# Optimization experiments

Hardware: AMD Instinct MI355X
Metric: run time of the kernel (lower is better)

Reference implementation:

```python
import jax, jax.numpy as jnp
import numpy as np

NUM_EMBEDDINGS = 1024
EMBEDDING_DIM = 128
COMMITMENT_COST = 1.0
DECAY = 0.99
EPSILON = 1e-05
N_TOKENS = 65536


def setup_inputs() -> dict:
    key = jax.random.key(0)
    k1, k2, k3 = jax.random.split(key, 3)
    inputs = jax.random.normal(k1, (N_TOKENS, EMBEDDING_DIM), dtype=jnp.float32)
    embedding = jax.random.normal(k2, (NUM_EMBEDDINGS, EMBEDDING_DIM), dtype=jnp.float32) * 0.01
    cluster_size = jnp.ones((NUM_EMBEDDINGS,), dtype=jnp.float32)
    embed_avg = jax.random.normal(k3, (NUM_EMBEDDINGS, EMBEDDING_DIM), dtype=jnp.float32) * 0.01
    return {"inputs": inputs, "embedding": embedding,
            "cluster_size": cluster_size, "embed_avg": embed_avg}


def reference(inputs, embedding, cluster_size, embed_avg):
    # inputs: [N, D], embedding: [K, D]
    flat = inputs.reshape(-1, EMBEDDING_DIM)
    distances = (jnp.sum(flat * flat, axis=1, keepdims=True)
                 + jnp.sum(embedding * embedding, axis=1)
                 - 2.0 * flat @ embedding.T)
    idx = jnp.argmin(distances, axis=1)                       # [N]
    quantized = embedding[idx].reshape(inputs.shape)          # direct gather (same math as one-hot matmul)

    # EMA update (training path); one-hot matmuls replaced by bincount/segment_sum
    dw = jnp.zeros((NUM_EMBEDDINGS,), dtype=flat.dtype).at[idx].add(1.0)   # encodings.sum(0)
    new_cluster_size = cluster_size * DECAY + (1.0 - DECAY) * dw
    dw_embed = jax.ops.segment_sum(flat, idx, num_segments=NUM_EMBEDDINGS)  # encodings.T @ flat
    new_embed_avg = embed_avg * DECAY + (1.0 - DECAY) * dw_embed
    n = jnp.sum(new_cluster_size)
    cs = (new_cluster_size + EPSILON) / (n + NUM_EMBEDDINGS * EPSILON) * n
    new_embedding = new_embed_avg / cs[:, None]

    # losses (quantized/inputs detach semantics are identical values in fwd)
    diff2 = jnp.mean((quantized - inputs) ** 2)
    loss = diff2 + COMMITMENT_COST * diff2

    # straight-through estimator: value equals quantized
    quantized_st = inputs + jax.lax.stop_gradient(quantized - inputs)
    return (quantized_st, loss, idx, new_embedding, new_cluster_size, new_embed_avg)
```

## Files before the change

kernel.cpp:

```cpp
#include <hip/hip_runtime.h>

typedef __attribute__((ext_vector_type(8))) _Float16 half8;
typedef __attribute__((ext_vector_type(4))) float f32x4;

constexpr int NTOK = 65536;
constexpr int DIM  = 128;
constexpr int NK   = 1024;

__global__ void bprep_k(const float* __restrict__ emb, char* __restrict__ bp,
                        float* __restrict__ embT, float* __restrict__ e2s,
                        double* __restrict__ en2d, int* __restrict__ nflag) {
  int i = blockIdx.x * 256 + threadIdx.x;
  if (i == 0) *nflag = 0;
  int c = i >> 4;
  int g = i & 15;
  float4 v0 = *(const float4*)&emb[c * 128 + g * 8];
  float4 v1 = *(const float4*)&emb[c * 128 + g * 8 + 4];
  float vf[8] = {v0.x, v0.y, v0.z, v0.w, v1.x, v1.y, v1.z, v1.w};
  half8 hv;
  double pacc = 0.0;
#pragma unroll
  for (int j = 0; j < 8; j++) {
    hv[j] = (_Float16)vf[j];
    embT[(g * 8 + j) * NK + c] = vf[j];
    pacc = fma((double)vf[j], (double)vf[j], pacc);
  }
  int chunk = c >> 5, n = (c >> 4) & 1, cl = c & 15;
  int kk = g >> 2, lo4 = g & 3;
  *(half8*)(bp + chunk * 8192 + kk * 2048 + n * 1024 + (lo4 * 16 + cl) * 16) = hv;
#pragma unroll
  for (int mask = 1; mask < 16; mask <<= 1) pacc += __shfl_xor(pacc, mask);
  if (g == 0) {
    en2d[c] = pacc;
    e2s[c] = (float)(pacc * 134217728.0 + 1073741824.0);
  }
}

__global__ __launch_bounds__(128, 2)
void argmin_k(const float* __restrict__ x, const char* __restrict__ bp,
              const float* __restrict__ e2s, int* __restrict__ idx_arr,
              float* __restrict__ out_idx, int* __restrict__ nflag,
              int* __restrict__ flags) {
  const int t    = threadIdx.x;
  const int lane = t & 63;
  const int w    = t >> 6;
  const int l15  = lane & 15;
  const int lo4  = lane >> 4;
  const int rbase = blockIdx.x * 64;
  const int lb16 = lane * 16;

  half8 FA[4][2], FB[4][2];

#define LOADG(DST, C, KK)                                                      \
  {                                                                            \
    const char* _b = bp + ((C) * 8192 + (KK) * 2048) + lb16;                   \
    DST[0] = *(const half8*)_b;                                                \
    DST[1] = *(const half8*)(_b + 1024);                                       \
  }

#pragma unroll
  for (int kk = 0; kk < 4; kk++) LOADG(FA[kk], 0, kk)
#pragma unroll
  for (int kk = 0; kk < 4; kk++) LOADG(FB[kk], 1, kk)

  half8 ah[2][4];
#pragma unroll
  for (int m = 0; m < 2; m++)
#pragma unroll
    for (int kk = 0; kk < 4; kk++) {
      const float* xp = &x[(rbase + w * 32 + m * 16 + l15) * 128 + kk * 32 + lo4 * 8];
      float4 v0 = *(const float4*)xp;
      float4 v1 = *(const float4*)(xp + 4);
      float vf[8] = {v0.x, v0.y, v0.z, v0.w, v1.x, v1.y, v1.z, v1.w};
      half8 av;
#pragma unroll
      for (int j = 0; j < 8; j++) av[j] = (_Float16)vf[j];
      ah[m][kk] = av;
    }

  unsigned bv[2][4], b2[2][4];
#pragma unroll
  for (int m = 0; m < 2; m++)
#pragma unroll
    for (int r = 0; r < 4; r++) { bv[m][r] = 0xFFFFFFFFu; b2[m][r] = 0xFFFFFFFFu; }

#define MFMA_PHASE(BANK, KK)                                                   \
  {                                                                            \
    acc[0][0] = __builtin_amdgcn_mfma_f32_16x16x32_f16(ah[0][KK], BANK[KK][0], acc[0][0], 0, 0, 0); \
    acc[1][0] = __builtin_amdgcn_mfma_f32_16x16x32_f16(ah[1][KK], BANK[KK][0], acc[1][0], 0, 0, 0); \
    acc[0][1] = __builtin_amdgcn_mfma_f32_16x16x32_f16(ah[0][KK], BANK[KK][1], acc[0][1], 0, 0, 0); \
    acc[1][1] = __builtin_amdgcn_mfma_f32_16x16x32_f16(ah[1][KK], BANK[KK][1], acc[1][1], 0, 0, 0); \
  }

#define KEY_EPI(C)                                                             \
  {                                                                            \
    _Pragma("unroll")                                                          \
    for (int n = 0; n < 2; n++) {                                              \
      unsigned col = (unsigned)((C) * 32 + n * 16 + l15);                      \
      float e2v = n ? e2b : e2a;                                               \
      _Pragma("unroll")                                                        \
      for (int m = 0; m < 2; m++)                                              \
        _Pragma("unroll")                                                      \
        for (int r = 0; r < 4; r++) {                                          \
          float ks = fmaf(acc[m][n][r], -268435456.0f, e2v);                   \
          unsigned key = ((unsigned)ks & 0xFFFFFC00u) | col;                   \
          unsigned old = bv[m][r];                                             \
          bv[m][r] = min(old, key);                                            \
          b2[m][r] = min(b2[m][r], max(old, key));                             \
        }                                                                      \
    }                                                                          \
  }

  for (int c = 0; c < 32; c += 2) {
    {
      float e2a = e2s[c * 32 + l15];
      float e2b = e2s[c * 32 + 16 + l15];
      f32x4 acc[2][2];
#pragma unroll
      for (int m = 0; m < 2; m++)
#pragma unroll
        for (int n = 0; n < 2; n++) acc[m][n] = (f32x4)(0.0f);
#pragma unroll
      for (int kk = 0; kk < 4; kk++) {
        MFMA_PHASE(FA, kk)
        LOADG(FA[kk], c + 2, kk)
      }
      KEY_EPI(c)
    }
    {
      float e2a = e2s[(c + 1) * 32 + l15];
      float e2b = e2s[(c + 1) * 32 + 16 + l15];
      f32x4 acc[2][2];
#pragma unroll
      for (int m = 0; m < 2; m++)
#pragma unroll
        for (int n = 0; n < 2; n++) acc[m][n] = (f32x4)(0.0f);
#pragma unroll
      for (int kk = 0; kk < 4; kk++) {
        MFMA_PHASE(FB, kk)
        LOADG(FB[kk], c + 3, kk)
      }
      KEY_EPI(c + 1)
    }
  }
#undef LOADG
#undef MFMA_PHASE
#undef KEY_EPI

#pragma unroll
  for (int m = 0; m < 2; m++)
#pragma unroll
    for (int r = 0; r < 4; r++) {
      unsigned v = bv[m][r], v2 = b2[m][r];
      for (int mask = 1; mask < 16; mask <<= 1) {
        unsigned ov = __shfl_xor(v, mask);
        unsigned o2 = __shfl_xor(v2, mask);
        v2 = min(min(v2, o2), max(v, ov));
        v  = min(v, ov);
      }
      if (l15 == 0) {
        int row = rbase + w * 32 + m * 16 + lo4 * 4 + r;
        int ii = (int)(v & 1023u);
        idx_arr[row] = ii;
        out_idx[row] = (float)ii;
        if ((v2 >> 10) - (v >> 10) < 79u) {
          int p = atomicAdd(nflag, 1); flags[p] = row;
        }
      }
    }
}

__global__ __launch_bounds__(256)
void fb_k(const float* __restrict__ x, const float* __restrict__ embT,
          const double* __restrict__ en2d, const int* __restrict__ nflag,
          const int* __restrict__ flags, int* __restrict__ idx_arr,
          float* __restrict__ out_idx) {
  int n = *nflag;
  __shared__ double xsh[4][DIM];
  __shared__ double sv[256];
  __shared__ int    si[256];
  int t = threadIdx.x;
  double n0 = en2d[t * 4 + 0], n1 = en2d[t * 4 + 1];
  double n2 = en2d[t * 4 + 2], n3 = en2d[t * 4 + 3];
  for (int base = blockIdx.x * 4; base < n; base += gridDim.x * 4) {
    int nb = min(4, n - base);
    __syncthreads();
    for (int u = t; u < nb * DIM; u += 256) {
      int j = u >> 7, d = u & 127;
      xsh[j][d] = (double)x[flags[base + j] * DIM + d];
    }
    __syncthreads();
    double xe[4][4];
#pragma unroll
    for (int j = 0; j < 4; j++)
#pragma unroll
      for (int q = 0; q < 4; q++) xe[j][q] = 0.0;
    for (int d = 0; d < DIM; d++) {
      float4 v = *(const float4*)&embT[d * NK + t * 4];
      double e0 = (double)v.x, e1 = (double)v.y, e2 = (double)v.z, e3 = (double)v.w;
#pragma unroll
      for (int j = 0; j < 4; j++) {
        double xd = xsh[j][d];
        xe[j][0] = fma(e0, xd, xe[j][0]);
        xe[j][1] = fma(e1, xd, xe[j][1]);
        xe[j][2] = fma(e2, xd, xe[j][2]);
        xe[j][3] = fma(e3, xd, xe[j][3]);
      }
    }
#pragma unroll
    for (int j = 0; j < 4; j++) {
      double s0 = n0 - 2.0 * xe[j][0];
      double s1 = n1 - 2.0 * xe[j][1];
      double s2 = n2 - 2.0 * xe[j][2];
      double s3 = n3 - 2.0 * xe[j][3];
      double bvv = s0; int bii = t * 4;
      if (s1 < bvv) { bvv = s1; bii = t * 4 + 1; }
      if (s2 < bvv) { bvv = s2; bii = t * 4 + 2; }
      if (s3 < bvv) { bvv = s3; bii = t * 4 + 3; }
      sv[t] = bvv; si[t] = bii;
      __syncthreads();
      for (int sh = 128; sh > 0; sh >>= 1) {
        if (t < sh) {
          double ov = sv[t + sh]; int oi = si[t + sh];
          if (ov < sv[t] || (ov == sv[t] && oi < si[t])) { sv[t] = ov; si[t] = oi; }
        }
        __syncthreads();
      }
      if (t == 0 && j < nb) {
        int row = flags[base + j];
        idx_arr[row] = si[0];
        out_idx[row] = (float)si[0];
      }
      __syncthreads();
    }
  }
}

__global__ void histb_k(const int* __restrict__ idx, unsigned* __restrict__ bcount) {
  __shared__ unsigned bins[NK];
  int t = threadIdx.x;
  for (int b = t; b < NK; b += 256) bins[b] = 0u;
  __syncthreads();
#pragma unroll
  for (int j = 0; j < 4; j++)
    atomicAdd(&bins[idx[blockIdx.x * 1024 + j * 256 + t]], 1u);
  __syncthreads();
  for (int b = t; b < NK; b += 256) bcount[blockIdx.x * NK + b] = bins[b];
}

__global__ void scan_k(unsigned* __restrict__ bcount, unsigned* __restrict__ icounts,
                       unsigned* __restrict__ offsets, const float* __restrict__ cs,
                       float* __restrict__ out_ncs, float* __restrict__ csk) {
  __shared__ unsigned sc[NK];
  __shared__ float sf[NK];
  int t = threadIdx.x;
  unsigned tot = 0;
#pragma unroll 8
  for (int b = 0; b < 64; b++) tot += bcount[b * NK + t];
  icounts[t] = tot;
  sc[t] = tot;
  __syncthreads();
  for (int off = 1; off < NK; off <<= 1) {
    unsigned v = (t >= off) ? sc[t - off] : 0u;
    __syncthreads();
    sc[t] += v;
    __syncthreads();
  }
  unsigned excl = sc[t] - tot;
  offsets[t] = excl;
  unsigned run = excl;
#pragma unroll 8
  for (int b = 0; b < 64; b++) {
    unsigned c = bcount[b * NK + t];
    bcount[b * NK + t] = run;
    run += c;
  }
  float c0 = cs[t];
  float ncs = c0 * 0.99f + 0.01f * (float)tot;
  out_ncs[t] = ncs;
  sf[t] = c0;
  __syncthreads();
  for (int s = 512; s > 0; s >>= 1) {
    if (t < s) sf[t] += sf[t + s];
    __syncthreads();
  }
  float n = 0.99f * sf[0] + 655.36f;
  csk[t] = (ncs + 1e-5f) / (n + 1024.0f * 1e-5f) * n;
}

__global__ void scatter_k(const int* __restrict__ idx, const unsigned* __restrict__ bstart,
                          int* __restrict__ order) {
  __shared__ unsigned cur[NK];
  int t = threadIdx.x;
  for (int b = t; b < NK; b += 256) cur[b] = bstart[blockIdx.x * NK + b];
  __syncthreads();
#pragma unroll
  for (int j = 0; j < 4; j++) {
    int r = blockIdx.x * 1024 + j * 256 + t;
    unsigned p = atomicAdd(&cur[idx[r]], 1u);
    order[p] = r;
  }
}

__global__ __launch_bounds__(512)
void fgather_k(const float* __restrict__ x, const float* __restrict__ emb,
               const unsigned* __restrict__ offsets, const unsigned* __restrict__ icounts,
               const int* __restrict__ order, float* __restrict__ out_q,
               float* __restrict__ dwsum2, float* __restrict__ partial2) {
  __shared__ int ids[1024];
  int k = blockIdx.x >> 1, half = blockIdx.x & 1;
  int t = threadIdx.x;
  int d = t & 127, h = t >> 7;
  unsigned cnt = icounts[k];
  unsigned chl = cnt >> 1;
  unsigned s = offsets[k] + (half ? chl : 0u);
  unsigned myc = half ? (cnt - chl) : chl;
  for (unsigned j = t; j < myc && j < 1024u; j += 512) ids[j] = order[s + j];
  __syncthreads();
  float e = emb[k * DIM + d];
  float acc = 0.f, ls = 0.f;
#pragma unroll 4
  for (unsigned j = h; j < myc; j += 4) {
    int row = (j < 1024u) ? ids[j] : order[s + j];
    float xv = x[row * DIM + d];
    out_q[row * DIM + d] = e;
    acc += xv;
    float dd = e - xv;
    ls += dd * dd;
  }
  __shared__ float sa[512], sl[512];
  sa[t] = acc; sl[t] = ls;
  __syncthreads();
  if (t < 128) dwsum2[(half * NK + k) * DIM + t] = sa[t] + sa[t + 128] + sa[t + 256] + sa[t + 384];
  for (int sh = 256; sh > 0; sh >>= 1) {
    if (t < sh) sl[t] += sl[t + sh];
    __syncthreads();
  }
  if (t == 0) partial2[blockIdx.x] = sl[0];
}

__global__ void emb_k(const float* __restrict__ embed_avg, const float* __restrict__ dwsum2,
                      const float* __restrict__ csk, const float* __restrict__ partial2,
                      float* __restrict__ out_nemb, float* __restrict__ out_nea,
                      float* __restrict__ out_loss) {
  if (blockIdx.x == 0) {
    __shared__ float red[256];
    int t = threadIdx.x;
    float v = 0.f;
#pragma unroll
    for (int i = 0; i < 8; i++) v += partial2[t + 256 * i];
    red[t] = v;
    __syncthreads();
    for (int sh = 128; sh > 0; sh >>= 1) {
      if (t < sh) red[t] += red[t + sh];
      __syncthreads();
    }
    if (t == 0) out_loss[0] = 2.0f * red[0] / 8388608.0f;
    return;
  }
  int i = (blockIdx.x - 1) * 256 + threadIdx.x;
  float dw = dwsum2[i] + dwsum2[NK * DIM + i];
  float na = embed_avg[i] * 0.99f + 0.01f * dw;
  out_nea[i] = na;
  out_nemb[i] = na / csk[i >> 7];
}

extern "C" void kernel_launch(void* const* d_in, const int* in_sizes, int n_in,
                              void* d_out, int out_size, void* d_ws, size_t ws_size,
                              hipStream_t stream) {
  const float* x   = (const float*)d_in[0];
  const float* emb = (const float*)d_in[1];
  const float* cs  = (const float*)d_in[2];
  const float* ea  = (const float*)d_in[3];

  float* out      = (float*)d_out;
  float* out_q    = out;
  float* out_loss = out + 8388608;
  float* out_idx  = out + 8388609;
  float* out_nemb = out + 8454145;
  float* out_ncs  = out + 8585217;
  float* out_nea  = out + 8586241;

  float* W        = (float*)d_ws;
  float* e2s      = W;
  double* en2d    = (double*)(W + 1024);
  char*  bpack    = (char*)(W + 3072);
  float* embT     = W + 134144;
  unsigned* bcount = (unsigned*)(W + 134144);
  int*   order    = (int*)(W + 199680);
  unsigned* icounts = (unsigned*)(W + 266240);
  unsigned* offsets = (unsigned*)(W + 267264);
  float* csk      = W + 268288;
  int*   nflag    = (int*)(W + 269312);
  int*   flags    = (int*)(W + 269328);
  int*   idx_arr  = (int*)(W + 334864);
  float* dwsum2   = W + 400400;
  float* partial2 = W + 662544;

  bprep_k<<<64, 256, 0, stream>>>(emb, bpack, embT, e2s, en2d, nflag);
  argmin_k<<<1024, 128, 0, stream>>>(x, bpack, e2s, idx_arr, out_idx, nflag, flags);
  fb_k<<<256, 256, 0, stream>>>(x, embT, en2d, nflag, flags, idx_arr, out_idx);
  histb_k<<<64, 256, 0, stream>>>(idx_arr, bcount);
  scan_k<<<1, 1024, 0, stream>>>(bcount, icounts, offsets, cs, out_ncs, csk);
  scatter_k<<<64, 256, 0, stream>>>(idx_arr, bcount, order);
  fgather_k<<<2048, 512, 0, stream>>>(x, emb, offsets, icounts, order, out_q, dwsum2, partial2);
  emb_k<<<513, 256, 0, stream>>>(ea, dwsum2, csk, partial2, out_nemb, out_nea, out_loss);
}
```

Before: 117.1 us.

## Split argmin codebook across two blocks and fuse histogram into merge kernel

The argmin kernel now gives each 64-row tile to two blocks, each scanning half the codebook, and raises the occupancy target in launch bounds. Each block writes its partial best and second-best keys. A new merge kernel combines the halves, writes indices, flags near-ties and builds the per-block histogram, which replaces the separate histogram kernel. The fallback kernel patches histogram counts when it changes an index, and scatter uses 1024-thread blocks. This aims to double the parallelism of the dominant distance kernel, at the cost of an extra partial-result round trip through global memory and more register pressure.

```diff
diff --git a/kernel.cpp b/kernel.cpp
--- a/kernel.cpp
+++ b/kernel.cpp
@@ -36,17 +36,19 @@
   }
 }
 
-__global__ __launch_bounds__(128, 2)
+__global__ __launch_bounds__(128, 4)
 void argmin_k(const float* __restrict__ x, const char* __restrict__ bp,
-              const float* __restrict__ e2s, int* __restrict__ idx_arr,
-              float* __restrict__ out_idx, int* __restrict__ nflag,
-              int* __restrict__ flags) {
+              const float* __restrict__ e2s, unsigned* __restrict__ bvh,
+              unsigned* __restrict__ b2h) {
   const int t    = threadIdx.x;
   const int lane = t & 63;
   const int w    = t >> 6;
   const int l15  = lane & 15;
   const int lo4  = lane >> 4;
-  const int rbase = blockIdx.x * 64;
+  const int rt   = blockIdx.x >> 1;
+  const int ch   = blockIdx.x & 1;
+  const int rbase = rt * 64;
+  const int cbase = ch * 16;
   const int lb16 = lane * 16;
 
   half8 FA[4][2], FB[4][2];
@@ -59,9 +61,9 @@
   }
 
 #pragma unroll
-  for (int kk = 0; kk < 4; kk++) LOADG(FA[kk], 0, kk)
-#pragma unroll
-  for (int kk = 0; kk < 4; kk++) LOADG(FB[kk], 1, kk)
+  for (int kk = 0; kk < 4; kk++) LOADG(FA[kk], cbase, kk)
+#pragma unroll
+  for (int kk = 0; kk < 4; kk++) LOADG(FB[kk], cbase + 1, kk)
 
   half8 ah[2][4];
 #pragma unroll
@@ -111,10 +113,11 @@
     }                                                                          \
   }
 
-  for (int c = 0; c < 32; c += 2) {
+  for (int i = 0; i < 16; i += 2) {
+    const int cg = cbase + i;
     {
-      float e2a = e2s[c * 32 + l15];
-      float e2b = e2s[c * 32 + 16 + l15];
+      float e2a = e2s[cg * 32 + l15];
+      float e2b = e2s[cg * 32 + 16 + l15];
       f32x4 acc[2][2];
 #pragma unroll
       for (int m = 0; m < 2; m++)
@@ -123,13 +126,13 @@
 #pragma unroll
       for (int kk = 0; kk < 4; kk++) {
         MFMA_PHASE(FA, kk)
-        LOADG(FA[kk], c + 2, kk)
-      }
-      KEY_EPI(c)
+        if (i + 2 < 16) LOADG(FA[kk], cg + 2, kk)
+      }
+      KEY_EPI(cg)
     }
     {
-      float e2a = e2s[(c + 1) * 32 + l15];
-      float e2b = e2s[(c + 1) * 32 + 16 + l15];
+      float e2a = e2s[(cg + 1) * 32 + l15];
+      float e2b = e2s[(cg + 1) * 32 + 16 + l15];
       f32x4 acc[2][2];
 #pragma unroll
       for (int m = 0; m < 2; m++)
@@ -138,9 +141,9 @@
 #pragma unroll
       for (int kk = 0; kk < 4; kk++) {
         MFMA_PHASE(FB, kk)
-        LOADG(FB[kk], c + 3, kk)
-      }
-      KEY_EPI(c + 1)
+        if (i + 3 < 16) LOADG(FB[kk], cg + 3, kk)
+      }
+      KEY_EPI(cg + 1)
     }
   }
 #undef LOADG
@@ -160,21 +163,41 @@
       }
       if (l15 == 0) {
         int row = rbase + w * 32 + m * 16 + lo4 * 4 + r;
-        int ii = (int)(v & 1023u);
-        idx_arr[row] = ii;
-        out_idx[row] = (float)ii;
-        if ((v2 >> 10) - (v >> 10) < 79u) {
-          int p = atomicAdd(nflag, 1); flags[p] = row;
-        }
-      }
-    }
+        bvh[ch * NTOK + row] = v;
+        b2h[ch * NTOK + row] = v2;
+      }
+    }
+}
+
+__global__ __launch_bounds__(1024)
+void merge_k(const unsigned* __restrict__ bvh, const unsigned* __restrict__ b2h,
+             int* __restrict__ idx_arr, float* __restrict__ out_idx,
+             int* __restrict__ nflag, int* __restrict__ flags,
+             unsigned* __restrict__ bcount) {
+  __shared__ unsigned bins[NK];
+  int t = threadIdx.x;
+  bins[t] = 0u;
+  __syncthreads();
+  int row = blockIdx.x * 1024 + t;
+  unsigned va = bvh[row], vb = bvh[NTOK + row];
+  unsigned v2 = min(min(b2h[row], b2h[NTOK + row]), max(va, vb));
+  unsigned v  = min(va, vb);
+  int ii = (int)(v & 1023u);
+  idx_arr[row] = ii;
+  out_idx[row] = (float)ii;
+  atomicAdd(&bins[ii], 1u);
+  if ((v2 >> 10) - (v >> 10) < 79u) {
+    int p = atomicAdd(nflag, 1); flags[p] = row;
+  }
+  __syncthreads();
+  bcount[blockIdx.x * NK + t] = bins[t];
 }
 
 __global__ __launch_bounds__(256)
 void fb_k(const float* __restrict__ x, const float* __restrict__ embT,
           const double* __restrict__ en2d, const int* __restrict__ nflag,
           const int* __restrict__ flags, int* __restrict__ idx_arr,
-          float* __restrict__ out_idx) {
+          float* __restrict__ out_idx, unsigned* __restrict__ bcount) {
   int n = *nflag;
   __shared__ double xsh[4][DIM];
   __shared__ double sv[256];
@@ -228,24 +251,19 @@
       }
       if (t == 0 && j < nb) {
         int row = flags[base + j];
-        idx_arr[row] = si[0];
-        out_idx[row] = (float)si[0];
+        int nw = si[0];
+        int old = idx_arr[row];
+        if (nw != old) {
+          idx_arr[row] = nw;
+          out_idx[row] = (float)nw;
+          int b = row >> 10;
+          atomicSub(&bcount[b * NK + old], 1u);
+          atomicAdd(&bcount[b * NK + nw], 1u);
+        }
       }
       __syncthreads();
     }
   }
-}
-
-__global__ void histb_k(const int* __restrict__ idx, unsigned* __restrict__ bcount) {
-  __shared__ unsigned bins[NK];
-  int t = threadIdx.x;
-  for (int b = t; b < NK; b += 256) bins[b] = 0u;
-  __syncthreads();
-#pragma unroll
-  for (int j = 0; j < 4; j++)
-    atomicAdd(&bins[idx[blockIdx.x * 1024 + j * 256 + t]], 1u);
-  __syncthreads();
-  for (int b = t; b < NK; b += 256) bcount[blockIdx.x * NK + b] = bins[b];
 }
 
 __global__ void scan_k(unsigned* __restrict__ bcount, unsigned* __restrict__ icounts,
@@ -288,18 +306,16 @@
   csk[t] = (ncs + 1e-5f) / (n + 1024.0f * 1e-5f) * n;
 }
 
-__global__ void scatter_k(const int* __restrict__ idx, const unsigned* __restrict__ bstart,
-                          int* __restrict__ order) {
+__global__ __launch_bounds__(1024)
+void scatter_k(const int* __restrict__ idx, const unsigned* __restrict__ bstart,
+               int* __restrict__ order) {
   __shared__ unsigned cur[NK];
   int t = threadIdx.x;
-  for (int b = t; b < NK; b += 256) cur[b] = bstart[blockIdx.x * NK + b];
-  __syncthreads();
-#pragma unroll
-  for (int j = 0; j < 4; j++) {
-    int r = blockIdx.x * 1024 + j * 256 + t;
-    unsigned p = atomicAdd(&cur[idx[r]], 1u);
-    order[p] = r;
-  }
+  cur[t] = bstart[blockIdx.x * NK + t];
+  __syncthreads();
+  int r = blockIdx.x * 1024 + t;
+  unsigned p = atomicAdd(&cur[idx[r]], 1u);
+  order[p] = r;
 }
 
 __global__ __launch_bounds__(512)
@@ -385,24 +401,26 @@
   float* e2s      = W;
   double* en2d    = (double*)(W + 1024);
   char*  bpack    = (char*)(W + 3072);
-  float* embT     = W + 134144;
-  unsigned* bcount = (unsigned*)(W + 134144);
-  int*   order    = (int*)(W + 199680);
-  unsigned* icounts = (unsigned*)(W + 266240);
-  unsigned* offsets = (unsigned*)(W + 267264);
-  float* csk      = W + 268288;
-  int*   nflag    = (int*)(W + 269312);
-  int*   flags    = (int*)(W + 269328);
-  int*   idx_arr  = (int*)(W + 334864);
-  float* dwsum2   = W + 400400;
-  float* partial2 = W + 662544;
+  float* embT     = W + 72704;
+  unsigned* bcount = (unsigned*)(W + 203776);
+  unsigned* icounts = (unsigned*)(W + 269312);
+  unsigned* offsets = (unsigned*)(W + 270336);
+  float* csk      = W + 271360;
+  int*   nflag    = (int*)(W + 272384);
+  int*   flags    = (int*)(W + 272400);
+  int*   idx_arr  = (int*)(W + 337936);
+  int*   order    = (int*)(W + 403472);
+  unsigned* bvh   = (unsigned*)(W + 469008);
+  unsigned* b2h   = (unsigned*)(W + 600080);
+  float* dwsum2   = W + 731152;
+  float* partial2 = W + 993296;
 
   bprep_k<<<64, 256, 0, stream>>>(emb, bpack, embT, e2s, en2d, nflag);
-  argmin_k<<<1024, 128, 0, stream>>>(x, bpack, e2s, idx_arr, out_idx, nflag, flags);
-  fb_k<<<256, 256, 0, stream>>>(x, embT, en2d, nflag, flags, idx_arr, out_idx);
-  histb_k<<<64, 256, 0, stream>>>(idx_arr, bcount);
+  argmin_k<<<2048, 128, 0, stream>>>(x, bpack, e2s, bvh, b2h);
+  merge_k<<<64, 1024, 0, stream>>>(bvh, b2h, idx_arr, out_idx, nflag, flags, bcount);
+  fb_k<<<256, 256, 0, stream>>>(x, embT, en2d, nflag, flags, idx_arr, out_idx, bcount);
   scan_k<<<1, 1024, 0, stream>>>(bcount, icounts, offsets, cs, out_ncs, csk);
-  scatter_k<<<64, 256, 0, stream>>>(idx_arr, bcount, order);
+  scatter_k<<<64, 1024, 0, stream>>>(idx_arr, bcount, order);
   fgather_k<<<2048, 512, 0, stream>>>(x, emb, offsets, icounts, order, out_q, dwsum2, partial2);
   emb_k<<<513, 256, 0, stream>>>(ea, dwsum2, csk, partial2, out_nemb, out_nea, out_loss);
 }
```

New measurement: 170.1 us. +45.3%, slower.
